# Optimization experiments

Hardware: AMD Instinct MI355X
Metric: run time of the kernel (lower is better)

## Reference

```python
import jax, jax.numpy as jnp
import numpy as np

# QuantizedLinear (BitNet-style ternary weights).
# The original pack_weights/unpack_weights 2-bit round-trip is an identity on the
# ternary values; the nested-loop ternary_matrix_operation is mathematically
# x @ Q^T (weights stored [out, in], accumulating +x[:,i] / -x[:,i] per +-1 entry).

def setup_inputs() -> dict:
    key = jax.random.key(0)
    k1, k2 = jax.random.split(key)
    TOKENS, IN_F, OUT_F = 8192, 4096, 4096
    x = jax.random.normal(k1, (TOKENS, IN_F), dtype=jnp.float32)
    weight = jax.random.normal(k2, (OUT_F, IN_F), dtype=jnp.float32)
    bias = jnp.zeros((OUT_F,), dtype=jnp.float32)
    return {"x": x, "weight": weight, "bias": bias}

def reference(x, weight, bias):
    # absmean ternary quantization: gamma = mean(|W|) + eps
    gamma = jnp.mean(jnp.abs(weight)) + 1e-5
    q = jnp.clip(jnp.round(weight / gamma), -1.0, 1.0)  # ternary {-1,0,1}, [out,in]
    # pack->unpack 2-bit round-trip is identity; loop accumulation == GEMM
    return jnp.einsum('bi,oi->bo', x, q) + bias
```

## Files before the change

kernel.cpp:

```cpp
#include <hip/hip_runtime.h>
#include <stdint.h>


#define M_DIM 8192
#define N_DIM 4096
#define K_DIM 4096
#define BM 128
#define BN 256
#define BK 64

typedef __attribute__((ext_vector_type(4))) int vi4;

#define BAR() asm volatile("s_barrier" ::: "memory")
#define VMW3() asm volatile("s_waitcnt vmcnt(3)" ::: "memory")
#define VMW0() asm volatile("s_waitcnt vmcnt(0)" ::: "memory")
#define SB0() __builtin_amdgcn_sched_barrier(0)
#define LGKM0()                                             \
  do {                                                      \
    SB0();                                                  \
    asm volatile("s_waitcnt lgkmcnt(0)" ::: "memory");      \
    SB0();                                                  \
  } while (0)

__device__ __forceinline__ void load_lds16(const void* g, void* l) {
  __builtin_amdgcn_global_load_lds(
      (const __attribute__((address_space(1))) void*)g,
      (__attribute__((address_space(3))) void*)l,
      16, 0, 0);
}

__global__ __launch_bounds__(256) void k_abs_partial(const float* __restrict__ w,
                                                     double* __restrict__ partial) {
  const int tid = threadIdx.x;
  const size_t base = (size_t)blockIdx.x * 8192 + (size_t)tid * 4;
  double s = 0.0;
#pragma unroll
  for (int it = 0; it < 8; ++it) {
    const float4 v = *reinterpret_cast<const float4*>(w + base + (size_t)it * 1024);
    s += (double)fabsf(v.x) + (double)fabsf(v.y) + (double)fabsf(v.z) + (double)fabsf(v.w);
  }
  __shared__ double sd[256];
  sd[tid] = s;
  __syncthreads();
  for (int off = 128; off > 0; off >>= 1) {
    if (tid < off) sd[tid] += sd[tid + off];
    __syncthreads();
  }
  if (tid == 0) partial[blockIdx.x] = sd[0];
}

__global__ __launch_bounds__(256) void k_abs_final(const double* __restrict__ partial,
                                                   float* __restrict__ gamma_out) {
  const int tid = threadIdx.x;
  double s = 0.0;
  for (int i = tid; i < 2048; i += 256) s += partial[i];
  __shared__ double sd[256];
  sd[tid] = s;
  __syncthreads();
  for (int off = 128; off > 0; off >>= 1) {
    if (tid < off) sd[tid] += sd[tid + off];
    __syncthreads();
  }
  if (tid == 0) {
    float g = (float)(sd[0] / 16777216.0);
    gamma_out[0] = g + 1e-5f;
  }
}

__global__ __launch_bounds__(256) void k_quant(const float* __restrict__ w,
                                               const float* __restrict__ gamma_p,
                                               int* __restrict__ qb) {
  const float g = gamma_p[0];
  const size_t n4 = (size_t)N_DIM * K_DIM / 4;
  const size_t stride = (size_t)gridDim.x * blockDim.x;
  for (size_t i = (size_t)blockIdx.x * blockDim.x + threadIdx.x; i < n4; i += stride) {
    const float4 v = reinterpret_cast<const float4*>(w)[i];
    float r;
    int a, b, c, d;
    r = rintf(v.x / g); a = (r >= 1.0f) ? 1 : ((r <= -1.0f) ? -1 : 0);
    r = rintf(v.y / g); b = (r >= 1.0f) ? 1 : ((r <= -1.0f) ? -1 : 0);
    r = rintf(v.z / g); c = (r >= 1.0f) ? 1 : ((r <= -1.0f) ? -1 : 0);
    r = rintf(v.w / g); d = (r >= 1.0f) ? 1 : ((r <= -1.0f) ? -1 : 0);
    qb[i] = (a & 0xff) | ((b & 0xff) << 8) | ((c & 0xff) << 16) | ((d & 0xff) << 24);
  }
}

__global__ __launch_bounds__(256) void k_quant_x(const float* __restrict__ x,
                                                 signed char* __restrict__ xq,
                                                 float* __restrict__ xs) {
  const int row = blockIdx.x;
  const int tid = threadIdx.x;
  const float* xr = x + (size_t)row * K_DIM;
  float4 v[4];
  float am = 0.0f;
#pragma unroll
  for (int i = 0; i < 4; ++i) {
    v[i] = reinterpret_cast<const float4*>(xr)[tid * 4 + i];
    am = fmaxf(am, fmaxf(fmaxf(fabsf(v[i].x), fabsf(v[i].y)),
                         fmaxf(fabsf(v[i].z), fabsf(v[i].w))));
  }
  for (int off = 32; off > 0; off >>= 1) am = fmaxf(am, __shfl_down(am, off));
  __shared__ float sm[4];
  if ((tid & 63) == 0) sm[tid >> 6] = am;
  __syncthreads();
  const float bm = fmaxf(fmaxf(fmaxf(sm[0], sm[1]), fmaxf(sm[2], sm[3])), 1e-20f);
  if (tid == 0) xs[row] = bm / 127.0f;
  const float inv = 127.0f / bm;
  union { signed char c[16]; int4 q; } u;
#pragma unroll
  for (int i = 0; i < 4; ++i) {
    u.c[i * 4 + 0] = (signed char)(int)rintf(v[i].x * inv);
    u.c[i * 4 + 1] = (signed char)(int)rintf(v[i].y * inv);
    u.c[i * 4 + 2] = (signed char)(int)rintf(v[i].z * inv);
    u.c[i * 4 + 3] = (signed char)(int)rintf(v[i].w * inv);
  }
  *reinterpret_cast<int4*>(xq + (size_t)row * K_DIM + tid * 16) = u.q;
}

__global__ __launch_bounds__(512, 4) void k_gemm(const signed char* __restrict__ Aq,
                                                 const signed char* __restrict__ Bq,
                                                 const float* __restrict__ xs,
                                                 const float* __restrict__ bias,
                                                 float* __restrict__ C) {
  __shared__ unsigned char lds[3][24576];

  const int tid = threadIdx.x;
  const int wid = tid >> 6;
  const int lane = tid & 63;
  const int wm = wid >> 2;
  const int wn = wid & 3;
  const int l15 = lane & 15;
  const int l4 = lane >> 4;

  const int c8 = blockIdx.x & 7;
  const int idx = blockIdx.x >> 3;
  const int bcol = (c8 * 2 + (idx & 1)) * BN;
  const int brow = (idx >> 1) * BM;

  const int srow = tid >> 2;
  const int scol = ((tid & 3) ^ ((tid >> 3) & 3)) << 4;
  const int rdoff = ((l4 ^ ((l15 >> 1) & 3)) << 4);

#define STAGE_ALL(buf, kt)                                                          \
  do {                                                                              \
    load_lds16(Aq + (size_t)(brow + srow) * K_DIM + (kt)*64 + scol,                 \
               (char*)&lds[buf][0] + (size_t)wid * 1024);                           \
    load_lds16(Bq + (size_t)(bcol + srow) * K_DIM + (kt)*64 + scol,                 \
               (char*)&lds[buf][8192] + (size_t)wid * 1024);                        \
    load_lds16(Bq + (size_t)(bcol + 128 + srow) * K_DIM + (kt)*64 + scol,           \
               (char*)&lds[buf][16384] + (size_t)wid * 1024);                       \
    SB0();                                                                          \
  } while (0)

#define RD8(buf)                                                                    \
  do {                                                                              \
    _Pragma("unroll") for (int i = 0; i < 4; ++i)                                   \
      fa[i] = *reinterpret_cast<const vi4*>(                                        \
          &lds[buf][0] + (size_t)(wm * 64 + i * 16 + l15) * 64 + rdoff);            \
    _Pragma("unroll") for (int p = 0; p < 4; ++p)                                   \
      fb[p] = *reinterpret_cast<const vi4*>(                                        \
          &lds[buf][8192] + (size_t)(wn * 64 + p * 16 + l15) * 64 + rdoff);         \
    SB0();                                                                          \
  } while (0)

#define MFMA16()                                                                    \
  do {                                                                              \
    __builtin_amdgcn_s_setprio(1);                                                  \
    _Pragma("unroll") for (int i = 0; i < 4; ++i)                                   \
      _Pragma("unroll") for (int p = 0; p < 4; ++p)                                 \
        acc[i][p] = __builtin_amdgcn_mfma_i32_16x16x64_i8(fa[i], fb[p],             \
                                                          acc[i][p], 0, 0, 0);      \
    __builtin_amdgcn_s_setprio(0);                                                  \
  } while (0)

  vi4 acc[4][4];
#pragma unroll
  for (int i = 0; i < 4; ++i)
#pragma unroll
    for (int p = 0; p < 4; ++p)
#pragma unroll
      for (int e = 0; e < 4; ++e) acc[i][p][e] = 0;

  vi4 fa[4], fb[4];

  STAGE_ALL(0, 0);
  STAGE_ALL(1, 1);
  VMW3();
  BAR();

  int cur = 0;
  for (int t = 0; t < 62; ++t) {
    const int stg = (cur == 0) ? 2 : cur - 1;
    RD8(cur);
    STAGE_ALL(stg, t + 2);
    LGKM0();
    MFMA16();
    VMW3();
    BAR();
    cur = (cur == 2) ? 0 : cur + 1;
  }
  RD8(cur);
  LGKM0();
  MFMA16();
  VMW0();
  BAR();
  RD8(0);
  LGKM0();
  MFMA16();

  float bi[4];
#pragma unroll
  for (int p = 0; p < 4; ++p) bi[p] = bias[bcol + wn * 64 + p * 16 + l15];
#pragma unroll
  for (int i = 0; i < 4; ++i) {
#pragma unroll
    for (int j = 0; j < 4; ++j) {
      const int row = brow + wm * 64 + i * 16 + l4 * 4 + j;
      const float sc = xs[row];
      float* crow = C + (size_t)row * N_DIM + bcol + wn * 64 + l15;
#pragma unroll
      for (int p = 0; p < 4; ++p) crow[p * 16] = (float)acc[i][p][j] * sc + bi[p];
    }
  }
#undef STAGE_ALL
#undef RD8
#undef MFMA16
}

extern "C" void kernel_launch(void* const* d_in, const int* in_sizes, int n_in,
                              void* d_out, int out_size, void* d_ws, size_t ws_size,
                              hipStream_t stream) {
  (void)in_sizes; (void)n_in; (void)out_size; (void)ws_size;
  const float* x = (const float*)d_in[0];
  const float* w = (const float*)d_in[1];
  const float* bias = (const float*)d_in[2];
  float* out = (float*)d_out;

  char* ws = (char*)d_ws;
  signed char* xq = (signed char*)ws;
  signed char* qb = (signed char*)(ws + (size_t)M_DIM * K_DIM);
  float* xs = (float*)(ws + (size_t)M_DIM * K_DIM + (size_t)N_DIM * K_DIM);
  double* partial = (double*)((char*)xs + M_DIM * sizeof(float));
  float* gamma = (float*)(partial + 2048);

  k_abs_partial<<<2048, 256, 0, stream>>>(w, partial);
  k_abs_final<<<1, 256, 0, stream>>>(partial, gamma);
  k_quant<<<2048, 256, 0, stream>>>(w, gamma, (int*)qb);
  k_quant_x<<<M_DIM, 256, 0, stream>>>(x, xq, xs);

  k_gemm<<<1024, 512, 0, stream>>>(xq, qb, xs, bias, out);
}
```

Before: 203.1 us.

## Halve GEMM workgroup to 4 waves, each computing a 64x128 tile

The int8 GEMM kernel drops from 8 waves per block to 4. Each wave now computes a 64x128 output sub-tile (32 MFMAs per k-step) instead of 64x64, and each thread issues 6 async global-to-LDS loads per stage, with the vmcnt wait adjusted to match. This raises the MFMA-to-LDS-read ratio per wave and cuts barrier participants, at the cost of doubling the accumulator registers, which lowers occupancy and gives fewer waves to hide latency.

Result: no change. 199.8 us (-1.6%).

```diff
diff --git a/kernel.cpp b/kernel.cpp
--- a/kernel.cpp
+++ b/kernel.cpp
@@ -12,7 +12,7 @@
 typedef __attribute__((ext_vector_type(4))) int vi4;
 
 #define BAR() asm volatile("s_barrier" ::: "memory")
-#define VMW3() asm volatile("s_waitcnt vmcnt(3)" ::: "memory")
+#define VMW6() asm volatile("s_waitcnt vmcnt(6)" ::: "memory")
 #define VMW0() asm volatile("s_waitcnt vmcnt(0)" ::: "memory")
 #define SB0() __builtin_amdgcn_sched_barrier(0)
 #define LGKM0()                                             \
@@ -117,7 +117,7 @@
   *reinterpret_cast<int4*>(xq + (size_t)row * K_DIM + tid * 16) = u.q;
 }
 
-__global__ __launch_bounds__(512, 4) void k_gemm(const signed char* __restrict__ Aq,
+__global__ __launch_bounds__(256, 2) void k_gemm(const signed char* __restrict__ Aq,
                                                  const signed char* __restrict__ Bq,
                                                  const float* __restrict__ xs,
                                                  const float* __restrict__ bias,
@@ -127,8 +127,8 @@
   const int tid = threadIdx.x;
   const int wid = tid >> 6;
   const int lane = tid & 63;
-  const int wm = wid >> 2;
-  const int wn = wid & 3;
+  const int wm = wid >> 1;
+  const int wn = wid & 1;
   const int l15 = lane & 15;
   const int l4 = lane >> 4;
 
@@ -143,88 +143,88 @@
 
 #define STAGE_ALL(buf, kt)                                                          \
   do {                                                                              \
-    load_lds16(Aq + (size_t)(brow + srow) * K_DIM + (kt)*64 + scol,                 \
-               (char*)&lds[buf][0] + (size_t)wid * 1024);                           \
-    load_lds16(Bq + (size_t)(bcol + srow) * K_DIM + (kt)*64 + scol,                 \
-               (char*)&lds[buf][8192] + (size_t)wid * 1024);                        \
-    load_lds16(Bq + (size_t)(bcol + 128 + srow) * K_DIM + (kt)*64 + scol,           \
-               (char*)&lds[buf][16384] + (size_t)wid * 1024);                       \
+    _Pragma("unroll") for (int a = 0; a < 2; ++a)                                   \
+      load_lds16(Aq + (size_t)(brow + a * 64 + srow) * K_DIM + (kt)*64 + scol,      \
+                 (char*)&lds[buf][0] + a * 4096 + (size_t)wid * 1024);              \
+    _Pragma("unroll") for (int b = 0; b < 4; ++b)                                   \
+      load_lds16(Bq + (size_t)(bcol + b * 64 + srow) * K_DIM + (kt)*64 + scol,      \
+                 (char*)&lds[buf][8192] + b * 4096 + (size_t)wid * 1024);           \
     SB0();                                                                          \
   } while (0)
 
-#define RD8(buf)                                                                    \
+#define RD12(buf)                                                                   \
   do {                                                                              \
     _Pragma("unroll") for (int i = 0; i < 4; ++i)                                   \
       fa[i] = *reinterpret_cast<const vi4*>(                                        \
           &lds[buf][0] + (size_t)(wm * 64 + i * 16 + l15) * 64 + rdoff);            \
-    _Pragma("unroll") for (int p = 0; p < 4; ++p)                                   \
+    _Pragma("unroll") for (int p = 0; p < 8; ++p)                                   \
       fb[p] = *reinterpret_cast<const vi4*>(                                        \
-          &lds[buf][8192] + (size_t)(wn * 64 + p * 16 + l15) * 64 + rdoff);         \
+          &lds[buf][8192] + (size_t)(wn * 128 + p * 16 + l15) * 64 + rdoff);        \
     SB0();                                                                          \
   } while (0)
 
-#define MFMA16()                                                                    \
+#define MFMA32()                                                                    \
   do {                                                                              \
     __builtin_amdgcn_s_setprio(1);                                                  \
     _Pragma("unroll") for (int i = 0; i < 4; ++i)                                   \
-      _Pragma("unroll") for (int p = 0; p < 4; ++p)                                 \
+      _Pragma("unroll") for (int p = 0; p < 8; ++p)                                 \
         acc[i][p] = __builtin_amdgcn_mfma_i32_16x16x64_i8(fa[i], fb[p],             \
                                                           acc[i][p], 0, 0, 0);      \
     __builtin_amdgcn_s_setprio(0);                                                  \
   } while (0)
 
-  vi4 acc[4][4];
+  vi4 acc[4][8];
 #pragma unroll
   for (int i = 0; i < 4; ++i)
 #pragma unroll
-    for (int p = 0; p < 4; ++p)
+    for (int p = 0; p < 8; ++p)
 #pragma unroll
       for (int e = 0; e < 4; ++e) acc[i][p][e] = 0;
 
-  vi4 fa[4], fb[4];
+  vi4 fa[4], fb[8];
 
   STAGE_ALL(0, 0);
   STAGE_ALL(1, 1);
-  VMW3();
+  VMW6();
   BAR();
 
   int cur = 0;
   for (int t = 0; t < 62; ++t) {
     const int stg = (cur == 0) ? 2 : cur - 1;
-    RD8(cur);
+    RD12(cur);
     STAGE_ALL(stg, t + 2);
     LGKM0();
-    MFMA16();
-    VMW3();
+    MFMA32();
+    VMW6();
     BAR();
     cur = (cur == 2) ? 0 : cur + 1;
   }
-  RD8(cur);
+  RD12(cur);
   LGKM0();
-  MFMA16();
+  MFMA32();
   VMW0();
   BAR();
-  RD8(0);
+  RD12(0);
   LGKM0();
-  MFMA16();
-
-  float bi[4];
-#pragma unroll
-  for (int p = 0; p < 4; ++p) bi[p] = bias[bcol + wn * 64 + p * 16 + l15];
+  MFMA32();
+
+  float bi[8];
+#pragma unroll
+  for (int p = 0; p < 8; ++p) bi[p] = bias[bcol + wn * 128 + p * 16 + l15];
 #pragma unroll
   for (int i = 0; i < 4; ++i) {
 #pragma unroll
     for (int j = 0; j < 4; ++j) {
       const int row = brow + wm * 64 + i * 16 + l4 * 4 + j;
       const float sc = xs[row];
-      float* crow = C + (size_t)row * N_DIM + bcol + wn * 64 + l15;
-#pragma unroll
-      for (int p = 0; p < 4; ++p) crow[p * 16] = (float)acc[i][p][j] * sc + bi[p];
+      float* crow = C + (size_t)row * N_DIM + bcol + wn * 128 + l15;
+#pragma unroll
+      for (int p = 0; p < 8; ++p) crow[p * 16] = (float)acc[i][p][j] * sc + bi[p];
     }
   }
 #undef STAGE_ALL
-#undef RD8
-#undef MFMA16
+#undef RD12
+#undef MFMA32
 }
 
 extern "C" void kernel_launch(void* const* d_in, const int* in_sizes, int n_in,
@@ -248,5 +248,5 @@
   k_quant<<<2048, 256, 0, stream>>>(w, gamma, (int*)qb);
   k_quant_x<<<M_DIM, 256, 0, stream>>>(x, xq, xs);
 
-  k_gemm<<<1024, 512, 0, stream>>>(xq, qb, xs, bias, out);
-}
+  k_gemm<<<1024, 256, 0, stream>>>(xq, qb, xs, bias, out);
+}
```
